# Performance work log

Hardware: AMD Instinct MI355X
Metric: run time of the kernel (lower is better)

The kernel has to match this reference:

```python
import jax, jax.numpy as jnp
import numpy as np
import math

EMBED_DIM = 1024
NUM_HEADS = 16
HEAD_DIM = EMBED_DIM // NUM_HEADS
B, S = 4, 2048


def setup_inputs() -> dict:
    key = jax.random.key(0)
    ks = jax.random.split(key, 12)
    sc = 1.0 / math.sqrt(EMBED_DIM)
    inp = {
        'query': jax.random.normal(ks[0], (B, S, EMBED_DIM), jnp.float32),
        'key': jax.random.normal(ks[1], (B, S, EMBED_DIM), jnp.float32),
        'value': jax.random.normal(ks[2], (B, S, EMBED_DIM), jnp.float32),
        # causal mask: 1 = attend, 0 = masked (matches masked_fill(attn_mask == 0, -inf))
        'attn_mask': jnp.tril(jnp.ones((S, S), jnp.int32)),
        'Wq': jax.random.normal(ks[3], (EMBED_DIM, EMBED_DIM), jnp.float32) * sc,
        'bq': jax.random.normal(ks[4], (EMBED_DIM,), jnp.float32) * sc,
        'Wk': jax.random.normal(ks[5], (EMBED_DIM, EMBED_DIM), jnp.float32) * sc,
        'bk': jax.random.normal(ks[6], (EMBED_DIM,), jnp.float32) * sc,
        'Wv': jax.random.normal(ks[7], (EMBED_DIM, EMBED_DIM), jnp.float32) * sc,
        'bv': jax.random.normal(ks[8], (EMBED_DIM,), jnp.float32) * sc,
        'Wo': jax.random.normal(ks[9], (EMBED_DIM, EMBED_DIM), jnp.float32) * sc,
        'bo': jax.random.normal(ks[10], (EMBED_DIM,), jnp.float32) * sc,
    }
    return inp


def reference(query, key, value, attn_mask, Wq, bq, Wk, bk, Wv, bv, Wo, bo):
    b, s, _ = query.shape
    # torch nn.Linear: x @ W.T + b
    q = (query @ Wq.T + bq).reshape(b, s, NUM_HEADS, HEAD_DIM)
    k = (key @ Wk.T + bk).reshape(b, s, NUM_HEADS, HEAD_DIM)
    v = (value @ Wv.T + bv).reshape(b, s, NUM_HEADS, HEAD_DIM)
    scores = jnp.einsum('bqhd,bkhd->bhqk', q, k) / math.sqrt(HEAD_DIM)
    neg_inf = jnp.asarray(-jnp.inf, scores.dtype)
    scores = jnp.where(attn_mask[None, None, :, :] == 0, neg_inf, scores)
    attn = jax.nn.softmax(scores, axis=-1)
    # dropout is identity in eval mode
    out = jnp.einsum('bhqk,bkhd->bqhd', attn, v).reshape(b, s, EMBED_DIM)
    return out @ Wo.T + bo
```

## Files before the change

kernel.cpp:

```cpp
#include <hip/hip_runtime.h>
#include <math.h>


#define EMBED 1024
#define SEQ   2048
#define NH    16
#define HD    64
#define QSCALE 0.18033688011112042f

typedef __attribute__((ext_vector_type(4))) float f32x4;
typedef __attribute__((ext_vector_type(8))) short s16x8;
typedef __attribute__((ext_vector_type(4))) short s16x4;
typedef __attribute__((ext_vector_type(4))) unsigned int u32x4;
typedef __attribute__((ext_vector_type(2))) unsigned int u32x2;

#define GLDS16(gp, lp) __builtin_amdgcn_global_load_lds( \
    (const __attribute__((address_space(1))) void*)(gp), \
    (__attribute__((address_space(3))) void*)(lp), 16, 0, 0)

__device__ __forceinline__ unsigned short f2bf(float f) {
    unsigned int u = __builtin_bit_cast(unsigned int, f);
    u += 0x7fffu + ((u >> 16) & 1u);
    return (unsigned short)(u >> 16);
}
__device__ __forceinline__ unsigned int pkbf(float lo, float hi) {
    return __builtin_amdgcn_perm(__builtin_bit_cast(unsigned int, hi),
                                 __builtin_bit_cast(unsigned int, lo),
                                 0x07060302u);
}

struct CvtArgs { const float* s[7]; unsigned short* d[7]; int n4[7]; };
__global__ void cvt_all(CvtArgs ca)
{
    const int t = blockIdx.y;
    const float* in = ca.s[t];
    unsigned short* out = ca.d[t];
    const int n4 = ca.n4[t];
    const int stride = gridDim.x * 256;
    for (int i = blockIdx.x * 256 + threadIdx.x; i < n4; i += stride) {
        f32x4 v = *(const f32x4*)(in + (size_t)i * 4);
        s16x4 p;
        p[0] = (short)f2bf(v[0]); p[1] = (short)f2bf(v[1]);
        p[2] = (short)f2bf(v[2]); p[3] = (short)f2bf(v[3]);
        *(s16x4*)(out + (size_t)i * 4) = p;
    }
}

struct ProjArgs {
    const unsigned short* X[3];
    const unsigned short* W[3];
    const float* Bz[3];
    unsigned short* Oz[3];
};
__global__ void __launch_bounds__(256)
gemm_qkv(ProjArgs pa)
{
    __shared__ unsigned short Ab[128 * 64];
    __shared__ unsigned short Bb[128 * 64];
    const int z = blockIdx.z;
    const unsigned short* Xb = pa.X[z];
    const unsigned short* Wb = pa.W[z];
    const float* bias = pa.Bz[z];
    unsigned short* Out = pa.Oz[z];
    const float scale = (z == 0) ? QSCALE : 1.0f;
    const int tid = threadIdx.x, lane = tid & 63, wv = tid >> 6;
    const int g = lane >> 4, c = lane & 15;
    const int wx = wv & 1, wy = wv >> 1;
    const int bm0 = blockIdx.x * 128, bn0 = blockIdx.y * 128;

    f32x4 acc[4][4];
#pragma unroll
    for (int i = 0; i < 4; ++i)
#pragma unroll
        for (int n = 0; n < 4; ++n) acc[i][n] = f32x4{0.f, 0.f, 0.f, 0.f};

    for (int k0 = 0; k0 < EMBED; k0 += 64) {
        __syncthreads();
#pragma unroll
        for (int cc = 0; cc < 4; ++cc) {
            int li = cc * 256 + tid;
            int row = li >> 3, ch = (li & 7) ^ (row & 7);
            GLDS16(Xb + (size_t)(bm0 + row) * EMBED + k0 + ch * 8,
                   Ab + cc * 2048 + wv * 512);
        }
#pragma unroll
        for (int cc = 0; cc < 4; ++cc) {
            int li = cc * 256 + tid;
            int row = li >> 3, ch = (li & 7) ^ (row & 7);
            GLDS16(Wb + (size_t)(bn0 + row) * EMBED + k0 + ch * 8,
                   Bb + cc * 2048 + wv * 512);
        }
        __syncthreads();
#pragma unroll
        for (int ks = 0; ks < 2; ++ks) {
            const int ib = ((ks * 4 + g) ^ (c & 7)) * 8;
            s16x8 af[4], bfr[4];
#pragma unroll
            for (int i = 0; i < 4; ++i)
                af[i] = *(const s16x8*)(&Ab[(wy * 64 + i * 16 + c) * 64 + ib]);
#pragma unroll
            for (int n = 0; n < 4; ++n)
                bfr[n] = *(const s16x8*)(&Bb[(wx * 64 + n * 16 + c) * 64 + ib]);
#pragma unroll
            for (int i = 0; i < 4; ++i)
#pragma unroll
                for (int n = 0; n < 4; ++n)
                    acc[i][n] = __builtin_amdgcn_mfma_f32_16x16x32_bf16(af[i], bfr[n], acc[i][n], 0, 0, 0);
        }
    }
    if (z < 2) {
#pragma unroll
        for (int i = 0; i < 4; ++i) {
            int m0 = bm0 + wy * 64 + i * 16 + g * 4;
            int bb = m0 >> 11, s0 = m0 & 2047;
#pragma unroll
            for (int n = 0; n < 4; ++n) {
                int ncol = bn0 + wx * 64 + n * 16 + c;
                float bv = bias[ncol];
                int hh = ncol >> 6, dd = ncol & 63;
                size_t base = (((size_t)bb * NH + hh) * SEQ + s0) * HD + dd;
#pragma unroll
                for (int r = 0; r < 4; ++r)
                    Out[base + (size_t)r * HD] = f2bf((acc[i][n][r] + bv) * scale);
            }
        }
    } else {
#pragma unroll
        for (int i = 0; i < 4; ++i) {
            int m0 = bm0 + wy * 64 + i * 16 + g * 4;
            int bb = m0 >> 11, s0 = m0 & 2047;
#pragma unroll
            for (int n = 0; n < 4; ++n) {
                int ncol = bn0 + wx * 64 + n * 16 + c;
                float bv = bias[ncol];
                int hh = ncol >> 6, dd = ncol & 63;
                s16x4 pk;
#pragma unroll
                for (int r = 0; r < 4; ++r) pk[r] = (short)f2bf(acc[i][n][r] + bv);
                *(s16x4*)(&Out[(((size_t)bb * NH + hh) * HD + dd) * SEQ + s0]) = pk;
            }
        }
    }
}

__global__ void __launch_bounds__(256)
gemm_out(const unsigned short* __restrict__ Xb, const unsigned short* __restrict__ Wb,
         const float* __restrict__ bias, float* __restrict__ Out)
{
    __shared__ unsigned short Ab[128 * 64];
    __shared__ unsigned short Bb[128 * 64];
    const int tid = threadIdx.x;
    const int lane = tid & 63, wv = tid >> 6;
    const int g = lane >> 4, c = lane & 15;
    const int wx = wv & 1, wy = wv >> 1;
    const int bm0 = blockIdx.x * 128, bn0 = blockIdx.y * 128;

    f32x4 acc[4][4];
#pragma unroll
    for (int i = 0; i < 4; ++i)
#pragma unroll
        for (int n = 0; n < 4; ++n) acc[i][n] = f32x4{0.f, 0.f, 0.f, 0.f};

    for (int k0 = 0; k0 < EMBED; k0 += 64) {
        __syncthreads();
#pragma unroll
        for (int cc = 0; cc < 4; ++cc) {
            int li = cc * 256 + tid;
            int row = li >> 3, ch = (li & 7) ^ (row & 7);
            GLDS16(Xb + (size_t)(bm0 + row) * EMBED + k0 + ch * 8,
                   Ab + cc * 2048 + wv * 512);
        }
#pragma unroll
        for (int cc = 0; cc < 4; ++cc) {
            int li = cc * 256 + tid;
            int row = li >> 3, ch = (li & 7) ^ (row & 7);
            GLDS16(Wb + (size_t)(bn0 + row) * EMBED + k0 + ch * 8,
                   Bb + cc * 2048 + wv * 512);
        }
        __syncthreads();
#pragma unroll
        for (int ks = 0; ks < 2; ++ks) {
            const int ib = ((ks * 4 + g) ^ (c & 7)) * 8;
            s16x8 af[4], bfr[4];
#pragma unroll
            for (int i = 0; i < 4; ++i)
                af[i] = *(const s16x8*)(&Ab[(wy * 64 + i * 16 + c) * 64 + ib]);
#pragma unroll
            for (int n = 0; n < 4; ++n)
                bfr[n] = *(const s16x8*)(&Bb[(wx * 64 + n * 16 + c) * 64 + ib]);
#pragma unroll
            for (int i = 0; i < 4; ++i)
#pragma unroll
                for (int n = 0; n < 4; ++n)
                    acc[i][n] = __builtin_amdgcn_mfma_f32_16x16x32_bf16(af[i], bfr[n], acc[i][n], 0, 0, 0);
        }
    }
#pragma unroll
    for (int i = 0; i < 4; ++i) {
#pragma unroll
        for (int n = 0; n < 4; ++n) {
            int ncol = bn0 + wx * 64 + n * 16 + c;
            float bv = bias[ncol];
#pragma unroll
            for (int r = 0; r < 4; ++r) {
                int m = bm0 + wy * 64 + i * 16 + g * 4 + r;
                Out[(size_t)m * EMBED + ncol] = acc[i][n][r] + bv;
            }
        }
    }
}

__global__ void __launch_bounds__(256)
attn_fwd(const unsigned short* __restrict__ Qb, const unsigned short* __restrict__ Kb,
         const unsigned short* __restrict__ Vg, unsigned short* __restrict__ Ob)
{
    __shared__ unsigned short Kt[2][64 * 64];
    __shared__ unsigned short Vt[2][64 * 64];
    __shared__ unsigned int   Pb[4][16 * 36];
    const int tid = threadIdx.x, lane = tid & 63, wv = tid >> 6;
    const int g = lane >> 4, c = lane & 15;
    const int h = blockIdx.y, b = blockIdx.z;
    const size_t bh = (size_t)b * NH + h;
    const unsigned short* K0 = Kb + bh * SEQ * HD;
    const unsigned short* V0 = Vg + bh * HD * SEQ;
    unsigned int* Pw = &Pb[wv][0];
    const int x0 = (g ^ (c & 7)) * 8;
    const int x1 = ((4 + g) ^ (c & 7)) * 8;
    const int li0 = tid, li1 = 256 + tid;
    const int kr0 = (li0 >> 3) * HD + (((li0 & 7) ^ ((li0 >> 3) & 7)) << 3);
    const int kr1 = (li1 >> 3) * HD + (((li1 & 7) ^ ((li1 >> 3) & 7)) << 3);
    const int vr0 = (li0 >> 3) * SEQ + (((li0 & 7) ^ ((li0 >> 3) & 7)) << 3);
    const int vr1 = (li1 >> 3) * SEQ + (((li1 & 7) ^ ((li1 >> 3) & 7)) << 3);

    for (int part = 0; part < 2; ++part) {
        const int qt = part ? blockIdx.x : (SEQ / 64 - 1 - blockIdx.x);
        const unsigned short* Qp = Qb + (bh * SEQ + qt * 64 + wv * 16) * HD;
        s16x8 qf0 = *(const s16x8*)(Qp + c * HD + g * 8);
        s16x8 qf1 = *(const s16x8*)(Qp + c * HD + 32 + g * 8);
        f32x4 o[4];
#pragma unroll
        for (int dt = 0; dt < 4; ++dt) o[dt] = f32x4{0.f, 0.f, 0.f, 0.f};
        float m_run = -INFINITY, l_run = 0.f;

        __syncthreads();
        {
            const unsigned short* Kg = K0;
            GLDS16(Kg + kr0, &Kt[0][0] + wv * 512);
            GLDS16(Kg + kr1, &Kt[0][2048] + wv * 512);
            GLDS16(V0 + vr0, &Vt[0][0] + wv * 512);
            GLDS16(V0 + vr1, &Vt[0][2048] + wv * 512);
        }

        for (int kt = 0; kt <= qt; ++kt) {
            __syncthreads();
            const int cur = kt & 1;
            if (kt < qt) {
                const int nxt = cur ^ 1;
                const unsigned short* Kg = K0 + (size_t)(kt + 1) * 64 * HD;
                GLDS16(Kg + kr0, &Kt[nxt][0] + wv * 512);
                GLDS16(Kg + kr1, &Kt[nxt][2048] + wv * 512);
                const unsigned short* Vp = V0 + (kt + 1) * 64;
                GLDS16(Vp + vr0, &Vt[nxt][0] + wv * 512);
                GLDS16(Vp + vr1, &Vt[nxt][2048] + wv * 512);
            }
            const unsigned short* Kc = &Kt[cur][0];
            const unsigned short* Vc = &Vt[cur][0];

            const int ntmax = (kt == qt) ? wv : 3;
            f32x4 sc[4];
#pragma unroll
            for (int nt = 0; nt < 4; ++nt) {
                if (nt <= ntmax) {
                    f32x4 a = f32x4{0.f, 0.f, 0.f, 0.f};
                    s16x8 kf0 = *(const s16x8*)(&Kc[(nt * 16 + c) * 64 + x0]);
                    s16x8 kf1 = *(const s16x8*)(&Kc[(nt * 16 + c) * 64 + x1]);
                    a = __builtin_amdgcn_mfma_f32_16x16x32_bf16(kf0, qf0, a, 0, 0, 0);
                    a = __builtin_amdgcn_mfma_f32_16x16x32_bf16(kf1, qf1, a, 0, 0, 0);
                    sc[nt] = a;
                } else {
                    sc[nt] = f32x4{-INFINITY, -INFINITY, -INFINITY, -INFINITY};
                }
            }
            if (kt == qt) {
#pragma unroll
                for (int nt = 0; nt < 4; ++nt)
#pragma unroll
                    for (int r = 0; r < 4; ++r)
                        if (nt * 16 + g * 4 + r > wv * 16 + c) sc[nt][r] = -INFINITY;
            }
            float mloc = -INFINITY;
#pragma unroll
            for (int nt = 0; nt < 4; ++nt)
                mloc = fmaxf(mloc, fmaxf(fmaxf(sc[nt][0], sc[nt][1]),
                                         fmaxf(sc[nt][2], sc[nt][3])));
            mloc = fmaxf(mloc, __shfl_xor(mloc, 16));
            mloc = fmaxf(mloc, __shfl_xor(mloc, 32));
            if (__any(mloc > m_run)) {
                float mnew = fmaxf(m_run, mloc);
                float alpha = __builtin_amdgcn_exp2f(m_run - mnew);
                m_run = mnew;
                l_run *= alpha;
                float av[4];
#pragma unroll
                for (int r = 0; r < 4; ++r) av[r] = __shfl(alpha, g * 4 + r, 16);
#pragma unroll
                for (int dt = 0; dt < 4; ++dt)
#pragma unroll
                    for (int r = 0; r < 4; ++r) o[dt][r] *= av[r];
            }
            float rs = 0.f;
#pragma unroll
            for (int nt = 0; nt < 4; ++nt)
#pragma unroll
                for (int r = 0; r < 4; ++r) {
                    float p = __builtin_amdgcn_exp2f(sc[nt][r] - m_run);
                    sc[nt][r] = p;
                    rs += p;
                }
            rs += __shfl_xor(rs, 16);
            rs += __shfl_xor(rs, 32);
            l_run += rs;
#pragma unroll
            for (int nt = 0; nt < 4; ++nt) {
                u32x2 w;
                w[0] = pkbf(sc[nt][0], sc[nt][1]);
                w[1] = pkbf(sc[nt][2], sc[nt][3]);
                *(u32x2*)(&Pw[c * 36 + nt * 8 + g * 2]) = w;
            }
#pragma unroll
            for (int kc = 0; kc < 2; ++kc) {
                s16x8 pf = *(const s16x8*)(&Pw[c * 36 + kc * 16 + g * 4]);
                const int xv = kc ? x1 : x0;
#pragma unroll
                for (int dt = 0; dt < 4; ++dt) {
                    s16x8 vf = *(const s16x8*)(&Vc[(dt * 16 + c) * 64 + xv]);
                    o[dt] = __builtin_amdgcn_mfma_f32_16x16x32_bf16(pf, vf, o[dt], 0, 0, 0);
                }
            }
        }
        float linv = 1.0f / l_run;
        float lv[4];
#pragma unroll
        for (int r = 0; r < 4; ++r) lv[r] = __shfl(linv, g * 4 + r, 16);
#pragma unroll
        for (int r = 0; r < 4; ++r) {
            int srow = qt * 64 + wv * 16 + g * 4 + r;
            size_t base = ((size_t)b * SEQ + srow) * EMBED + h * HD;
#pragma unroll
            for (int dt = 0; dt < 4; ++dt)
                Ob[base + dt * 16 + c] = f2bf(o[dt][r] * lv[r]);
        }
    }
}

extern "C" void kernel_launch(void* const* d_in, const int* in_sizes, int n_in,
                              void* d_out, int out_size, void* d_ws, size_t ws_size,
                              hipStream_t stream)
{
    (void)in_sizes; (void)n_in; (void)out_size; (void)ws_size;
    const float* Xq = (const float*)d_in[0];
    const float* Xk = (const float*)d_in[1];
    const float* Xv = (const float*)d_in[2];
    const float* Wq = (const float*)d_in[4];
    const float* bq = (const float*)d_in[5];
    const float* Wk = (const float*)d_in[6];
    const float* bk = (const float*)d_in[7];
    const float* Wv = (const float*)d_in[8];
    const float* bv = (const float*)d_in[9];
    const float* Wo = (const float*)d_in[10];
    const float* bo = (const float*)d_in[11];
    float* Out = (float*)d_out;

    unsigned short* ws = (unsigned short*)d_ws;
    unsigned short* wqb = ws;
    unsigned short* wkb = wqb + 1048576;
    unsigned short* wvb = wkb + 1048576;
    unsigned short* wob = wvb + 1048576;
    unsigned short* xqb = wob + 1048576;
    unsigned short* xkb = xqb + 8388608;
    unsigned short* xvb = xkb + 8388608;
    unsigned short* Qb  = xvb + 8388608;
    unsigned short* Kb  = Qb + 8388608;
    unsigned short* Vb  = Kb + 8388608;
    unsigned short* Ax  = xqb;

    CvtArgs ca;
    ca.s[0] = Wq; ca.s[1] = Wk; ca.s[2] = Wv; ca.s[3] = Wo;
    ca.s[4] = Xq; ca.s[5] = Xk; ca.s[6] = Xv;
    ca.d[0] = wqb; ca.d[1] = wkb; ca.d[2] = wvb; ca.d[3] = wob;
    ca.d[4] = xqb; ca.d[5] = xkb; ca.d[6] = xvb;
    ca.n4[0] = ca.n4[1] = ca.n4[2] = ca.n4[3] = 262144;
    ca.n4[4] = ca.n4[5] = ca.n4[6] = 2097152;
    cvt_all<<<dim3(2048, 7), 256, 0, stream>>>(ca);

    ProjArgs pa;
    pa.X[0] = xqb; pa.X[1] = xkb; pa.X[2] = xvb;
    pa.W[0] = wqb; pa.W[1] = wkb; pa.W[2] = wvb;
    pa.Bz[0] = bq; pa.Bz[1] = bk; pa.Bz[2] = bv;
    pa.Oz[0] = Qb; pa.Oz[1] = Kb; pa.Oz[2] = Vb;
    gemm_qkv<<<dim3(64, 8, 3), 256, 0, stream>>>(pa);

    attn_fwd<<<dim3(16, NH, 4), 256, 0, stream>>>(Qb, Kb, Vb, Ax);

    gemm_out<<<dim3(64, 8), 256, 0, stream>>>(Ax, wob, bo, Out);
}
```

Before: 354.3 us.

## Load V fragments directly from global into registers, drop V LDS buffer

The attention kernel no longer stages V tiles through double-buffered shared memory. Each wave reads its V fragments straight from global memory (V is stored transposed per head) into registers at the start of every key tile. A minimum-occupancy launch bound is added, relying on the smaller LDS footprint. The cost is that all four waves read the same V data redundantly from global/L2, with no prefetch ahead of use, which can expose load latency on the PV MFMAs.

```diff
diff --git a/kernel.cpp b/kernel.cpp
--- a/kernel.cpp
+++ b/kernel.cpp
@@ -210,12 +210,11 @@
     }
 }
 
-__global__ void __launch_bounds__(256)
+__global__ void __launch_bounds__(256, 4)
 attn_fwd(const unsigned short* __restrict__ Qb, const unsigned short* __restrict__ Kb,
          const unsigned short* __restrict__ Vg, unsigned short* __restrict__ Ob)
 {
     __shared__ unsigned short Kt[2][64 * 64];
-    __shared__ unsigned short Vt[2][64 * 64];
     __shared__ unsigned int   Pb[4][16 * 36];
     const int tid = threadIdx.x, lane = tid & 63, wv = tid >> 6;
     const int g = lane >> 4, c = lane & 15;
@@ -229,8 +228,7 @@
     const int li0 = tid, li1 = 256 + tid;
     const int kr0 = (li0 >> 3) * HD + (((li0 & 7) ^ ((li0 >> 3) & 7)) << 3);
     const int kr1 = (li1 >> 3) * HD + (((li1 & 7) ^ ((li1 >> 3) & 7)) << 3);
-    const int vr0 = (li0 >> 3) * SEQ + (((li0 & 7) ^ ((li0 >> 3) & 7)) << 3);
-    const int vr1 = (li1 >> 3) * SEQ + (((li1 & 7) ^ ((li1 >> 3) & 7)) << 3);
+    const unsigned short* Vrow = V0 + (size_t)c * SEQ + g * 8;
 
     for (int part = 0; part < 2; ++part) {
         const int qt = part ? blockIdx.x : (SEQ / 64 - 1 - blockIdx.x);
@@ -244,27 +242,28 @@
 
         __syncthreads();
         {
-            const unsigned short* Kg = K0;
-            GLDS16(Kg + kr0, &Kt[0][0] + wv * 512);
-            GLDS16(Kg + kr1, &Kt[0][2048] + wv * 512);
-            GLDS16(V0 + vr0, &Vt[0][0] + wv * 512);
-            GLDS16(V0 + vr1, &Vt[0][2048] + wv * 512);
+            GLDS16(K0 + kr0, &Kt[0][0] + wv * 512);
+            GLDS16(K0 + kr1, &Kt[0][2048] + wv * 512);
         }
 
         for (int kt = 0; kt <= qt; ++kt) {
             __syncthreads();
             const int cur = kt & 1;
             if (kt < qt) {
-                const int nxt = cur ^ 1;
                 const unsigned short* Kg = K0 + (size_t)(kt + 1) * 64 * HD;
-                GLDS16(Kg + kr0, &Kt[nxt][0] + wv * 512);
-                GLDS16(Kg + kr1, &Kt[nxt][2048] + wv * 512);
-                const unsigned short* Vp = V0 + (kt + 1) * 64;
-                GLDS16(Vp + vr0, &Vt[nxt][0] + wv * 512);
-                GLDS16(Vp + vr1, &Vt[nxt][2048] + wv * 512);
+                GLDS16(Kg + kr0, &Kt[cur ^ 1][0] + wv * 512);
+                GLDS16(Kg + kr1, &Kt[cur ^ 1][2048] + wv * 512);
+            }
+            s16x8 vfr[2][4];
+            {
+                const unsigned short* Vk = Vrow + kt * 64;
+#pragma unroll
+                for (int kc = 0; kc < 2; ++kc)
+#pragma unroll
+                    for (int dt = 0; dt < 4; ++dt)
+                        vfr[kc][dt] = *(const s16x8*)(Vk + (size_t)(dt * 16) * SEQ + kc * 32);
             }
             const unsigned short* Kc = &Kt[cur][0];
-            const unsigned short* Vc = &Vt[cur][0];
 
             const int ntmax = (kt == qt) ? wv : 3;
             f32x4 sc[4];
@@ -330,12 +329,9 @@
 #pragma unroll
             for (int kc = 0; kc < 2; ++kc) {
                 s16x8 pf = *(const s16x8*)(&Pw[c * 36 + kc * 16 + g * 4]);
-                const int xv = kc ? x1 : x0;
-#pragma unroll
-                for (int dt = 0; dt < 4; ++dt) {
-                    s16x8 vf = *(const s16x8*)(&Vc[(dt * 16 + c) * 64 + xv]);
-                    o[dt] = __builtin_amdgcn_mfma_f32_16x16x32_bf16(pf, vf, o[dt], 0, 0, 0);
-                }
+#pragma unroll
+                for (int dt = 0; dt < 4; ++dt)
+                    o[dt] = __builtin_amdgcn_mfma_f32_16x16x32_bf16(pf, vfr[kc][dt], o[dt], 0, 0, 0);
             }
         }
         float linv = 1.0f / l_run;
```

Result: slower. 397.2 us (+12.1%).

## Share K/V tiles across two query tiles in 512-thread attention blocks

Applied to the files above, without the earlier changes.

The attention kernel now runs 8 waves per block: two groups of four waves, each group handling one of two adjacent 64-row query tiles. Each K/V tile loaded into shared memory serves both query tiles, which halves K/V global and LDS load traffic per query row and halves the grid size. Query tile pairs are chosen as jj and 15-jj to keep the causal work balanced across blocks. In exchange, the first query group's waves sit idle on the last key tile. The launch bounds (512, 4) may also cap registers tightly enough to cause spills or lower occupancy.

```diff
diff --git a/kernel.cpp b/kernel.cpp
--- a/kernel.cpp
+++ b/kernel.cpp
@@ -210,15 +210,16 @@
     }
 }
 
-__global__ void __launch_bounds__(256)
+__global__ void __launch_bounds__(512, 4)
 attn_fwd(const unsigned short* __restrict__ Qb, const unsigned short* __restrict__ Kb,
          const unsigned short* __restrict__ Vg, unsigned short* __restrict__ Ob)
 {
     __shared__ unsigned short Kt[2][64 * 64];
     __shared__ unsigned short Vt[2][64 * 64];
-    __shared__ unsigned int   Pb[4][16 * 36];
+    __shared__ unsigned int   Pb[8][16 * 36];
     const int tid = threadIdx.x, lane = tid & 63, wv = tid >> 6;
     const int g = lane >> 4, c = lane & 15;
+    const int wq = wv >> 2, wr = wv & 3;
     const int h = blockIdx.y, b = blockIdx.z;
     const size_t bh = (size_t)b * NH + h;
     const unsigned short* K0 = Kb + bh * SEQ * HD;
@@ -226,15 +227,15 @@
     unsigned int* Pw = &Pb[wv][0];
     const int x0 = (g ^ (c & 7)) * 8;
     const int x1 = ((4 + g) ^ (c & 7)) * 8;
-    const int li0 = tid, li1 = 256 + tid;
-    const int kr0 = (li0 >> 3) * HD + (((li0 & 7) ^ ((li0 >> 3) & 7)) << 3);
-    const int kr1 = (li1 >> 3) * HD + (((li1 & 7) ^ ((li1 >> 3) & 7)) << 3);
-    const int vr0 = (li0 >> 3) * SEQ + (((li0 & 7) ^ ((li0 >> 3) & 7)) << 3);
-    const int vr1 = (li1 >> 3) * SEQ + (((li1 & 7) ^ ((li1 >> 3) & 7)) << 3);
+    const int srow = tid >> 3, sch = (tid & 7) ^ (srow & 7);
+    const int kr = srow * HD + sch * 8;
+    const int vr = srow * SEQ + sch * 8;
 
     for (int part = 0; part < 2; ++part) {
-        const int qt = part ? blockIdx.x : (SEQ / 64 - 1 - blockIdx.x);
-        const unsigned short* Qp = Qb + (bh * SEQ + qt * 64 + wv * 16) * HD;
+        const int jj = part ? (15 - blockIdx.x) : blockIdx.x;
+        const int qt = 2 * jj + wq;
+        const int kmax = 2 * jj + 1;
+        const unsigned short* Qp = Qb + (bh * SEQ + qt * 64 + wr * 16) * HD;
         s16x8 qf0 = *(const s16x8*)(Qp + c * HD + g * 8);
         s16x8 qf1 = *(const s16x8*)(Qp + c * HD + 32 + g * 8);
         f32x4 o[4];
@@ -244,29 +245,22 @@
 
         __syncthreads();
         {
-            const unsigned short* Kg = K0;
-            GLDS16(Kg + kr0, &Kt[0][0] + wv * 512);
-            GLDS16(Kg + kr1, &Kt[0][2048] + wv * 512);
-            GLDS16(V0 + vr0, &Vt[0][0] + wv * 512);
-            GLDS16(V0 + vr1, &Vt[0][2048] + wv * 512);
-        }
-
-        for (int kt = 0; kt <= qt; ++kt) {
+            GLDS16(K0 + kr, &Kt[0][0] + wv * 512);
+            GLDS16(V0 + vr, &Vt[0][0] + wv * 512);
+        }
+
+        for (int kt = 0; kt <= kmax; ++kt) {
             __syncthreads();
             const int cur = kt & 1;
-            if (kt < qt) {
-                const int nxt = cur ^ 1;
-                const unsigned short* Kg = K0 + (size_t)(kt + 1) * 64 * HD;
-                GLDS16(Kg + kr0, &Kt[nxt][0] + wv * 512);
-                GLDS16(Kg + kr1, &Kt[nxt][2048] + wv * 512);
-                const unsigned short* Vp = V0 + (kt + 1) * 64;
-                GLDS16(Vp + vr0, &Vt[nxt][0] + wv * 512);
-                GLDS16(Vp + vr1, &Vt[nxt][2048] + wv * 512);
-            }
+            if (kt < kmax) {
+                GLDS16(K0 + (size_t)(kt + 1) * 64 * HD + kr, &Kt[cur ^ 1][0] + wv * 512);
+                GLDS16(V0 + (kt + 1) * 64 + vr, &Vt[cur ^ 1][0] + wv * 512);
+            }
+            if (kt > qt) continue;
             const unsigned short* Kc = &Kt[cur][0];
             const unsigned short* Vc = &Vt[cur][0];
 
-            const int ntmax = (kt == qt) ? wv : 3;
+            const int ntmax = (kt == qt) ? wr : 3;
             f32x4 sc[4];
 #pragma unroll
             for (int nt = 0; nt < 4; ++nt) {
@@ -286,7 +280,7 @@
                 for (int nt = 0; nt < 4; ++nt)
 #pragma unroll
                     for (int r = 0; r < 4; ++r)
-                        if (nt * 16 + g * 4 + r > wv * 16 + c) sc[nt][r] = -INFINITY;
+                        if (nt * 16 + g * 4 + r > wr * 16 + c) sc[nt][r] = -INFINITY;
             }
             float mloc = -INFINITY;
 #pragma unroll
@@ -344,8 +338,8 @@
         for (int r = 0; r < 4; ++r) lv[r] = __shfl(linv, g * 4 + r, 16);
 #pragma unroll
         for (int r = 0; r < 4; ++r) {
-            int srow = qt * 64 + wv * 16 + g * 4 + r;
-            size_t base = ((size_t)b * SEQ + srow) * EMBED + h * HD;
+            int sr = qt * 64 + wr * 16 + g * 4 + r;
+            size_t base = ((size_t)b * SEQ + sr) * EMBED + h * HD;
 #pragma unroll
             for (int dt = 0; dt < 4; ++dt)
                 Ob[base + dt * 16 + c] = f2bf(o[dt][r] * lv[r]);
@@ -400,7 +394,7 @@
     pa.Oz[0] = Qb; pa.Oz[1] = Kb; pa.Oz[2] = Vb;
     gemm_qkv<<<dim3(64, 8, 3), 256, 0, stream>>>(pa);
 
-    attn_fwd<<<dim3(16, NH, 4), 256, 0, stream>>>(Qb, Kb, Vb, Ax);
+    attn_fwd<<<dim3(8, NH, 4), 512, 0, stream>>>(Qb, Kb, Vb, Ax);
 
     gemm_out<<<dim3(64, 8), 256, 0, stream>>>(Ax, wob, bo, Out);
 }
```

New measurement: 331.5 us. -6.4%, faster.
